# Kernel tuning notes

Hardware: AMD Instinct MI355X
Metric: run time of the kernel (lower is better)

## Reference

```python
import jax, jax.numpy as jnp
import numpy as np

TAU = 2.0       # LIF time constant
ALPHA = 4.0     # spikingjelly Sigmoid surrogate alpha
EPS = 1e-5      # BatchNorm eps
NUM_HEADS = 8

@jax.custom_vjp
def _spike(x):
    return (x >= 0.0).astype(x.dtype)

def _spike_fwd(x):
    return _spike(x), x

def _spike_bwd(x, g):
    s = jax.nn.sigmoid(ALPHA * x)
    return (g * ALPHA * s * (1.0 - s),)

_spike.defvjp(_spike_fwd, _spike_bwd)

def lif(x, v_th=1.0):
    """Multi-step LIF over leading time axis. v <- v + (x - v)/tau; hard reset to 0.
    detach_reset=True: spike in reset path is stop-gradient'ed."""
    def step(v, xt):
        v = v + (xt - v) / TAU
        s = _spike(v - v_th)
        v = v * (1.0 - jax.lax.stop_gradient(s))
        return v, s
    _, out = jax.lax.scan(step, jnp.zeros_like(x[0]), x)
    return out

def conv_bn(x, w, gamma, beta, mean, var, bias=None):
    """1x1 Conv1d over channel dim + BatchNorm1d (inference-style, running stats).
    x: [T,B,C,N], w: [Cout,Cin]."""
    y = jnp.einsum('tbcn,dc->tbdn', x, w)
    if bias is not None:
        y = y + bias[None, None, :, None]
    inv = gamma * jax.lax.rsqrt(var + EPS)
    return (y - mean[None, None, :, None]) * inv[None, None, :, None] + beta[None, None, :, None]

def _bn_params(key, C):
    k1, k2, k3 = jax.random.split(key, 3)
    gamma = 1.0 + 0.1 * jax.random.normal(k1, (C,), jnp.float32)
    beta = 0.1 * jax.random.normal(k2, (C,), jnp.float32)
    mean = 0.1 * jax.random.normal(k3, (C,), jnp.float32)
    var = jnp.ones((C,), jnp.float32)
    return gamma, beta, mean, var

def setup_inputs() -> dict:
    key = jax.random.key(0)
    ks = jax.random.split(key, 10)
    T, B, C, N = 4, 8, 512, 1024
    scale = 1.0 / np.sqrt(C)
    d = {}
    d['q'] = jax.random.normal(ks[0], (T, B, C, N), jnp.float32)
    d['k'] = jax.random.normal(ks[1], (T, B, C, N), jnp.float32)
    d['q_w'] = jax.random.normal(ks[2], (C, C), jnp.float32) * scale
    d['k_w'] = jax.random.normal(ks[3], (C, C), jnp.float32) * scale
    d['proj_w'] = jax.random.normal(ks[4], (C, C), jnp.float32) * scale
    d['proj_b'] = 0.01 * jax.random.normal(ks[5], (C,), jnp.float32)
    d['q_gamma'], d['q_beta'], d['q_mean'], d['q_var'] = _bn_params(ks[6], C)
    d['k_gamma'], d['k_beta'], d['k_mean'], d['k_var'] = _bn_params(ks[7], C)
    d['proj_gamma'], d['proj_beta'], d['proj_mean'], d['proj_var'] = _bn_params(ks[8], C)
    return d

def reference(q, k, q_w, k_w, proj_w, proj_b,
              q_gamma, q_beta, q_mean, q_var,
              k_gamma, k_beta, k_mean, k_var,
              proj_gamma, proj_beta, proj_mean, proj_var):
    T, B, C, N = q.shape
    H = NUM_HEADS
    Dh = C // H
    # Q path: conv1x1 + BN + LIF spikes, split heads
    q_s = lif(conv_bn(q, q_w, q_gamma, q_beta, q_mean, q_var))          # [T,B,C,N]
    q_h = q_s.reshape(T, B, H, Dh, N)
    # K path
    k_s = lif(conv_bn(k, k_w, k_gamma, k_beta, k_mean, k_var))          # [T,B,C,N]
    k_h = k_s.reshape(T, B, H, Dh, N)
    # Sum-pool Q over head_dim, spike-gate (threshold 0.5), multiply into K
    q_sum = jnp.sum(q_h, axis=3, keepdims=True)                         # [T,B,H,1,N]
    attn = lif(q_sum, v_th=0.5)                                         # [T,B,H,1,N]
    x = (attn * k_h).reshape(T, B, C, N)
    # Projection: conv1x1 (with bias) + BN + LIF
    x = conv_bn(x, proj_w, proj_gamma, proj_beta, proj_mean, proj_var, bias=proj_b)
    return lif(x)
```

## Files before the change

### kernel.cpp

```cpp
#include <hip/hip_runtime.h>
#include <hip/hip_fp16.h>
#include <stdint.h>

#define TT 4
#define BB 8
#define CC 512
#define NN 1024
#define HH 8

typedef unsigned char u8;
typedef _Float16 f16x8 __attribute__((ext_vector_type(8)));
typedef float f32x16 __attribute__((ext_vector_type(16)));

#define WF_BYTES ((size_t)2*64*512*16)
#define SZ_SPIKE ((size_t)TT*BB*CC*NN)
#define SZ_GATE  ((size_t)TT*BB*HH*NN)

union U4H { uint4 u; f16x8 v; };
__device__ __forceinline__ f16x8 ash(uint4 u){ U4H x; x.u = u; return x.v; }

#define MFMA_F16(a,b,c) __builtin_amdgcn_mfma_f32_32x32x16_f16((a),(b),(c),0,0,0)

__device__ __forceinline__ void gld_lds16(const void* g, void* l){
  __builtin_amdgcn_global_load_lds((const __attribute__((address_space(1))) void*)g,
                                   (__attribute__((address_space(3))) void*)l, 16, 0, 0);
}
__device__ __forceinline__ void gld_lds4(const void* g, void* l){
  __builtin_amdgcn_global_load_lds((const __attribute__((address_space(1))) void*)g,
                                   (__attribute__((address_space(3))) void*)l, 4, 0, 0);
}

#define WAITVM(N) asm volatile("s_waitcnt vmcnt(" #N ")" ::: "memory")
#define WAITLGKM0 asm volatile("s_waitcnt lgkmcnt(0)" ::: "memory")
#define SBAR() __builtin_amdgcn_s_barrier()
#define VMFENCE() asm volatile("" ::: "memory")

__device__ __forceinline__ void split16(float xs, uint32_t& h, uint32_t& m){
  __half hh = __float2half(xs);
  float hf = __half2float(hh);
  __half mm = __float2half(xs - hf);
  h = __half_as_ushort(hh);
  m = __half_as_ushort(mm);
}

__global__ __launch_bounds__(256)
void k_prep(const float* __restrict__ W0, const float* __restrict__ W1,
            const float* __restrict__ W2,
            u8* __restrict__ D0, u8* __restrict__ D1, u8* __restrict__ D2)
{
  const int which = blockIdx.y;
  const float* W = (which == 0) ? W0 : (which == 1) ? W1 : W2;
  u8* D = (which == 0) ? D0 : (which == 1) ? D1 : D2;
  const int tg  = blockIdx.x * 256 + threadIdx.x;
  const int row = tg >> 6;
  const int kh  = tg & 63;
  uint32_t Hw[4], Mw[4];
#pragma unroll
  for (int p = 0; p < 4; ++p){
    uint32_t h0, m0, h1, m1;
    split16(W[row * CC + kh * 8 + 2*p    ] * 64.0f, h0, m0);
    split16(W[row * CC + kh * 8 + 2*p + 1] * 64.0f, h1, m1);
    Hw[p] = h0 | (h1 << 16);
    Mw[p] = m0 | (m1 << 16);
  }
  *(uint4*)(D + ((size_t)(0*64 + kh)*512 + row) * 16) = make_uint4(Hw[0],Hw[1],Hw[2],Hw[3]);
  *(uint4*)(D + ((size_t)(1*64 + kh)*512 + row) * 16) = make_uint4(Mw[0],Mw[1],Mw[2],Mw[3]);
}

__global__ __launch_bounds__(256, 2)
void k_qk(const float* __restrict__ Q, const float* __restrict__ K,
          const u8* __restrict__ WFq, const u8* __restrict__ WFk,
          const float* __restrict__ qg, const float* __restrict__ qb,
          const float* __restrict__ qm, const float* __restrict__ qv,
          const float* __restrict__ kg, const float* __restrict__ kb,
          const float* __restrict__ km, const float* __restrict__ kv,
          u8* __restrict__ Sk, u8* __restrict__ Aa)
{
  __shared__ float xf32[3][4096];
  __shared__ uint4 frag[1024];

  const int hw = blockIdx.x;
  const int lg = (hw & 7) * 128 + (hw >> 3);
  const int d0t  = lg & 1;
  const int n0i  = (lg >> 1) & 31;
  const int b    = (lg >> 6) & 7;
  const int path = (lg >> 9) & 1;
  const int n0 = n0i << 5, d0 = d0t << 8;
  const float* X = path ? K : Q;
  const u8* WF = path ? WFk : WFq;

  const int tid = threadIdx.x, lane = tid & 63, wid = tid >> 6;
  const int hi = lane >> 5, ln31 = lane & 31;

  f32x16 acc[4][2];
#pragma unroll
  for (int t = 0; t < 4; ++t)
#pragma unroll
    for (int rt = 0; rt < 2; ++rt)
#pragma unroll
      for (int r = 0; r < 16; ++r) acc[t][rt][r] = 0.0f;

  uint4 A0[8], A1[8];

  auto stageX = [&](int h, int buf){
    const float* xb = X + ((size_t)(wid*BB + b)*CC + h*32)*NN + n0;
#pragma unroll
    for (int i = 0; i < 4; ++i){
      gld_lds16(xb + (size_t)(i*8 + (lane >> 3))*NN + ((lane & 7) << 2),
                (void*)&xf32[buf][(wid*32 + i*8)*32]);
    }
  };
  auto loadA = [&](uint4* A, int h){
#pragma unroll
    for (int s = 0; s < 2; ++s)
#pragma unroll
      for (int ks = 0; ks < 2; ++ks)
#pragma unroll
        for (int rt = 0; rt < 2; ++rt)
          A[s*4 + ks*2 + rt] = *(const uint4*)(WF +
              ((size_t)(s*64 + h*4 + ks*2 + hi)*512
               + d0 + wid*64 + rt*32 + ln31) * 16);
  };
  auto dosplit = [&](int sb){
    const int c = tid & 127;
    const int t = c >> 5, n = c & 31;
    const int k0 = (tid >> 7) << 4;
    const float* xs = &xf32[sb][(t*32 + k0)*32 + n];
    uint32_t hw_[8], mw_[8];
#pragma unroll
    for (int p = 0; p < 8; ++p){
      uint32_t ha, ma, hb2, mb2;
      split16(xs[(2*p  )*32] * 512.0f, ha, ma);
      split16(xs[(2*p+1)*32] * 512.0f, hb2, mb2);
      hw_[p] = ha | (hb2 << 16);
      mw_[p] = ma | (mb2 << 16);
    }
    const int kb0 = k0 >> 3;
    frag[(kb0    )*128 + c] = make_uint4(hw_[0],hw_[1],hw_[2],hw_[3]);
    frag[(kb0 + 1)*128 + c] = make_uint4(hw_[4],hw_[5],hw_[6],hw_[7]);
    frag[(4 + kb0    )*128 + c] = make_uint4(mw_[0],mw_[1],mw_[2],mw_[3]);
    frag[(4 + kb0 + 1)*128 + c] = make_uint4(mw_[4],mw_[5],mw_[6],mw_[7]);
  };
  auto mstep = [&](const uint4* A){
#pragma unroll
    for (int ks = 0; ks < 2; ++ks){
      const int kbi = ks*2 + hi;
#pragma unroll
      for (int ct = 0; ct < 4; ++ct){
        const int fb = ct*32 + ln31;
        f16x8 bh = ash(frag[kbi*128 + fb]);
        f16x8 bm = ash(frag[(4 + kbi)*128 + fb]);
#pragma unroll
        for (int rt = 0; rt < 2; ++rt){
          acc[ct][rt] = MFMA_F16(ash(A[0*4 + ks*2 + rt]), bh, acc[ct][rt]);
          acc[ct][rt] = MFMA_F16(ash(A[1*4 + ks*2 + rt]), bh, acc[ct][rt]);
          acc[ct][rt] = MFMA_F16(ash(A[0*4 + ks*2 + rt]), bm, acc[ct][rt]);
        }
      }
    }
  };

#define QK_PH(H, VM) { \
    WAITVM(VM); SBAR(); \
    if ((H) < 15) { loadA(((H)&1) ? A0 : A1, (H)+1); VMFENCE(); } \
    if ((H) < 14) { stageX((H)+2, ((H)+2)%3); VMFENCE(); } \
    dosplit((H)%3); \
    WAITLGKM0; SBAR(); \
    mstep(((H)&1) ? A1 : A0); }

  stageX(0, 0); VMFENCE(); stageX(1, 1); VMFENCE(); loadA(A0, 0);
  QK_PH(0,12)  QK_PH(1,12)  QK_PH(2,12)  QK_PH(3,12)
  QK_PH(4,12)  QK_PH(5,12)  QK_PH(6,12)  QK_PH(7,12)
  QK_PH(8,12)  QK_PH(9,12)  QK_PH(10,12) QK_PH(11,12)
  QK_PH(12,12) QK_PH(13,12) QK_PH(14,12) QK_PH(15,8)
#undef QK_PH

  const float* gamma = path ? kg : qg;
  const float* beta  = path ? kb : qb;
  const float* mean  = path ? km : qm;
  const float* var   = path ? kv : qv;

  uint32_t orb = 0;
#pragma unroll
  for (int rt = 0; rt < 2; ++rt)
#pragma unroll
    for (int rg = 0; rg < 4; ++rg){
      const int dbase = d0 + wid*64 + rt*32 + rg*8 + hi*4;
      const float4 g4 = *(const float4*)&gamma[dbase];
      const float4 b4 = *(const float4*)&beta[dbase];
      const float4 m4 = *(const float4*)&mean[dbase];
      const float4 v4 = *(const float4*)&var[dbase];
      const float* gp = (const float*)&g4;
      const float* bp = (const float*)&b4;
      const float* mp = (const float*)&m4;
      const float* vp = (const float*)&v4;
#pragma unroll
      for (int j = 0; j < 4; ++j){
        const float inv = gp[j] * (1.0f / sqrtf(vp[j] + 1e-5f));
        const float c1 = inv * (1.0f/32768.0f);
        const float c0 = bp[j] - mp[j]*inv;
        const int r = rg*4 + j;
        float v = 0.f;
#pragma unroll
        for (int t = 0; t < 4; ++t){
          const float y = fmaf(acc[t][rt][r], c1, c0);
          v = 0.5f*(v + y);
          const bool s = (v >= 1.0f);
          if (s) v = 0.f;
          if (path == 1)
            Sk[((size_t)(t*BB + b)*CC + dbase + j)*NN + n0 + ln31] = (u8)s;
          else
            orb |= ((uint32_t)s) << t;
        }
      }
    }

  if (path == 0){
    orb |= __shfl_xor(orb, 32);
    if (hi == 0){
      const int h = d0t*4 + wid;
#pragma unroll
      for (int t = 0; t < 4; ++t)
        Aa[((size_t)(t*BB + b)*HH + h)*NN + n0 + ln31] = (u8)((orb >> t) & 1);
    }
  }
}

__global__ __launch_bounds__(256, 2)
void k_proj(const u8* __restrict__ Sk, const u8* __restrict__ Ag,
            const u8* __restrict__ WF, const float* __restrict__ bias,
            const float* __restrict__ gamma, const float* __restrict__ beta,
            const float* __restrict__ mean, const float* __restrict__ var,
            float* __restrict__ O)
{
  __shared__ u8   xu[3][8192];
  __shared__ uint4 frag[1024];

  const int hw = blockIdx.x;
  const int lg = (hw & 7) * 64 + (hw >> 3);
  const int d0t = lg & 1;
  const int n0i = (lg >> 1) & 31;
  const int b   = (lg >> 6) & 7;
  const int n0 = n0i << 5, d0 = d0t << 8;

  const int tid = threadIdx.x, lane = tid & 63, wid = tid >> 6;
  const int hi = lane >> 5, ln31 = lane & 31;

  const int st_kh = tid >> 5, st_t = (tid >> 3) & 3, st_n4 = tid & 7;

  f32x16 acc[4][2];
#pragma unroll
  for (int t = 0; t < 4; ++t)
#pragma unroll
    for (int rt = 0; rt < 2; ++rt)
#pragma unroll
      for (int r = 0; r < 16; ++r) acc[t][rt][r] = 0.0f;

  uint4 Ap[16];
  uint32_t gword[8];
#pragma unroll
  for (int p = 0; p < 8; ++p)
    gword[p] = *(const uint32_t*)(Ag +
        ((size_t)(st_t*BB + b)*HH + p)*NN + n0 + st_n4*4);

  auto xustage = [&](int h, int buf){
#pragma unroll
    for (int i = 0; i < 8; ++i){
      const u8* g = Sk + ((size_t)((wid*BB + b)*CC) + (size_t)(h*64 + i*8 + (lane >> 3)))*NN
                       + n0 + (lane & 7)*4;
      gld_lds4(g, (void*)&xu[buf][(wid*64 + i*8)*32]);
    }
  };
  auto loadPA = [&](int p){
#pragma unroll
    for (int s = 0; s < 2; ++s)
#pragma unroll
      for (int ks = 0; ks < 4; ++ks)
#pragma unroll
        for (int rt = 0; rt < 2; ++rt)
          Ap[(s*4 + ks)*2 + rt] = *(const uint4*)(WF +
              ((size_t)(s*64 + p*8 + ks*2 + hi)*512
               + d0 + wid*64 + rt*32 + ln31) * 16);
  };
  auto stage2 = [&](int buf, uint32_t g32){
    uint32_t r[8];
#pragma unroll
    for (int c = 0; c < 8; ++c)
      r[c] = *(const uint32_t*)&xu[buf][(st_t*64 + st_kh*8 + c)*32 + st_n4*4];
#pragma unroll
    for (int j = 0; j < 4; ++j){
      const uint32_t gm   = __builtin_amdgcn_perm(g32, g32, (uint32_t)j * 0x01010101u);
      const uint32_t selp = (uint32_t)j | (((uint32_t)j + 4u) << 8);
      uint32_t p01 = __builtin_amdgcn_perm(r[1], r[0], selp);
      uint32_t p23 = __builtin_amdgcn_perm(r[3], r[2], selp);
      uint32_t p45 = __builtin_amdgcn_perm(r[5], r[4], selp);
      uint32_t p67 = __builtin_amdgcn_perm(r[7], r[6], selp);
      uint32_t lo  = __builtin_amdgcn_perm(p23, p01, 0x05040100u) & gm;
      uint32_t hi_ = __builtin_amdgcn_perm(p67, p45, 0x05040100u) & gm;
      uint32_t w[4];
#pragma unroll
      for (int p = 0; p < 4; ++p){
        const uint32_t src = (p < 2) ? lo : hi_;
        const uint32_t b0 = (src >> ((p & 1) * 16)) & 0xFFu;
        const uint32_t b1 = (src >> ((p & 1) * 16 + 8)) & 0xFFu;
        w[p] = (b0 ? 0x3C00u : 0u) | (b1 ? 0x3C000000u : 0u);
      }
      frag[st_kh*128 + st_t*32 + st_n4*4 + j] = make_uint4(w[0], w[1], w[2], w[3]);
    }
  };
  auto mstepP = [&](){
#pragma unroll
    for (int ks = 0; ks < 4; ++ks){
      const int kbi = ks*2 + hi;
#pragma unroll
      for (int ct = 0; ct < 4; ++ct){
        const int fb = ct*32 + ln31;
        f16x8 bb = ash(frag[kbi*128 + fb]);
#pragma unroll
        for (int rt = 0; rt < 2; ++rt){
          acc[ct][rt] = MFMA_F16(ash(Ap[(0*4 + ks)*2 + rt]), bb, acc[ct][rt]);
          acc[ct][rt] = MFMA_F16(ash(Ap[(1*4 + ks)*2 + rt]), bb, acc[ct][rt]);
        }
      }
    }
  };

#define PJ_PH(P, VM) { \
    WAITVM(VM); SBAR(); \
    loadPA(P); VMFENCE(); \
    if ((P) < 6) { xustage((P)+2, ((P)+2)%3); VMFENCE(); } \
    stage2((P)%3, gword[P]); \
    WAITLGKM0; SBAR(); \
    mstepP(); }

  xustage(0, 0); VMFENCE(); xustage(1, 1); VMFENCE();
  PJ_PH(0,8) PJ_PH(1,8) PJ_PH(2,8) PJ_PH(3,8)
  PJ_PH(4,8) PJ_PH(5,8) PJ_PH(6,8) PJ_PH(7,0)
#undef PJ_PH

#pragma unroll
  for (int rt = 0; rt < 2; ++rt)
#pragma unroll
    for (int rg = 0; rg < 4; ++rg){
      const int dbase = d0 + wid*64 + rt*32 + rg*8 + hi*4;
      const float4 g4 = *(const float4*)&gamma[dbase];
      const float4 b4 = *(const float4*)&beta[dbase];
      const float4 m4 = *(const float4*)&mean[dbase];
      const float4 v4 = *(const float4*)&var[dbase];
      const float4 s4 = *(const float4*)&bias[dbase];
      const float* gp = (const float*)&g4;
      const float* bp = (const float*)&b4;
      const float* mp = (const float*)&m4;
      const float* vp = (const float*)&v4;
      const float* sp = (const float*)&s4;
#pragma unroll
      for (int j = 0; j < 4; ++j){
        const float inv = gp[j] * (1.0f / sqrtf(vp[j] + 1e-5f));
        const float c1 = inv * (1.0f/64.0f);
        const float c0 = (sp[j] - mp[j])*inv + bp[j];
        const int r = rg*4 + j;
        float v = 0.f;
#pragma unroll
        for (int t = 0; t < 4; ++t){
          const float y = fmaf(acc[t][rt][r], c1, c0);
          v = 0.5f*(v + y);
          const bool s = (v >= 1.0f);
          if (s) v = 0.f;
          O[((size_t)(t*BB + b)*CC + dbase + j)*NN + n0 + ln31] = s ? 1.f : 0.f;
        }
      }
    }
}

extern "C" void kernel_launch(void* const* d_in, const int* in_sizes, int n_in,
                              void* d_out, int out_size, void* d_ws, size_t ws_size,
                              hipStream_t stream)
{
  const float* q   = (const float*)d_in[0];
  const float* k   = (const float*)d_in[1];
  const float* qw  = (const float*)d_in[2];
  const float* kw  = (const float*)d_in[3];
  const float* pw  = (const float*)d_in[4];
  const float* pb  = (const float*)d_in[5];
  const float* qg  = (const float*)d_in[6];
  const float* qbt = (const float*)d_in[7];
  const float* qm  = (const float*)d_in[8];
  const float* qv  = (const float*)d_in[9];
  const float* kg  = (const float*)d_in[10];
  const float* kbt = (const float*)d_in[11];
  const float* km  = (const float*)d_in[12];
  const float* kv  = (const float*)d_in[13];
  const float* pg  = (const float*)d_in[14];
  const float* pbt = (const float*)d_in[15];
  const float* pm  = (const float*)d_in[16];
  const float* pv  = (const float*)d_in[17];

  u8* WFq = (u8*)d_ws;
  u8* WFk = WFq + WF_BYTES;
  u8* WFp = WFk + WF_BYTES;
  u8* Sk  = WFp + WF_BYTES;
  u8* Aa  = Sk + SZ_SPIKE;
  const size_t need = 3*WF_BYTES + SZ_SPIKE + SZ_GATE;
  if (ws_size < need) return;

  k_prep<<<dim3(128, 3), 256, 0, stream>>>(qw, kw, pw, WFq, WFk, WFp);
  k_qk<<<1024, 256, 0, stream>>>(q, k, WFq, WFk,
                                 qg, qbt, qm, qv, kg, kbt, km, kv, Sk, Aa);
  k_proj<<<512, 256, 0, stream>>>(Sk, Aa, WFp, pb, pg, pbt, pm, pv, (float*)d_out);
}
```

Baseline: 163.5 us.

## Widen QK tile to all 512 output channels and load X through registers

Each block of the Q/K conv kernel now computes all 512 output channels for its 32-column slice, instead of splitting the channels across two blocks. This halves the grid and means each X element is read and split into f16 parts only once rather than twice. The LDS fp32 staging via global_load_lds is replaced by direct per-thread global loads into registers, a double-buffered fragment array, and a simpler one-barrier-per-phase pipeline. The accumulator count doubles and occupancy is lowered to one block per CU, so latency hiding may suffer and the register-loaded strided X reads may coalesce worse.

```diff
diff --git a/kernel.cpp b/kernel.cpp
--- a/kernel.cpp
+++ b/kernel.cpp
@@ -21,10 +21,6 @@
 
 #define MFMA_F16(a,b,c) __builtin_amdgcn_mfma_f32_32x32x16_f16((a),(b),(c),0,0,0)
 
-__device__ __forceinline__ void gld_lds16(const void* g, void* l){
-  __builtin_amdgcn_global_load_lds((const __attribute__((address_space(1))) void*)g,
-                                   (__attribute__((address_space(3))) void*)l, 16, 0, 0);
-}
 __device__ __forceinline__ void gld_lds4(const void* g, void* l){
   __builtin_amdgcn_global_load_lds((const __attribute__((address_space(1))) void*)g,
                                    (__attribute__((address_space(3))) void*)l, 4, 0, 0);
@@ -67,7 +63,7 @@
   *(uint4*)(D + ((size_t)(1*64 + kh)*512 + row) * 16) = make_uint4(Mw[0],Mw[1],Mw[2],Mw[3]);
 }
 
-__global__ __launch_bounds__(256, 2)
+__global__ __launch_bounds__(256, 1)
 void k_qk(const float* __restrict__ Q, const float* __restrict__ K,
           const u8* __restrict__ WFq, const u8* __restrict__ WFk,
           const float* __restrict__ qg, const float* __restrict__ qb,
@@ -76,103 +72,103 @@
           const float* __restrict__ km, const float* __restrict__ kv,
           u8* __restrict__ Sk, u8* __restrict__ Aa)
 {
-  __shared__ float xf32[3][4096];
-  __shared__ uint4 frag[1024];
+  __shared__ uint4 frag[2][1024];
 
   const int hw = blockIdx.x;
-  const int lg = (hw & 7) * 128 + (hw >> 3);
-  const int d0t  = lg & 1;
-  const int n0i  = (lg >> 1) & 31;
-  const int b    = (lg >> 6) & 7;
-  const int path = (lg >> 9) & 1;
-  const int n0 = n0i << 5, d0 = d0t << 8;
+  const int lg = (hw & 7) * 64 + (hw >> 3);
+  const int n0i  = lg & 31;
+  const int b    = (lg >> 5) & 7;
+  const int path = (lg >> 8) & 1;
+  const int n0 = n0i << 5;
   const float* X = path ? K : Q;
   const u8* WF = path ? WFk : WFq;
 
   const int tid = threadIdx.x, lane = tid & 63, wid = tid >> 6;
   const int hi = lane >> 5, ln31 = lane & 31;
 
-  f32x16 acc[4][2];
-#pragma unroll
-  for (int t = 0; t < 4; ++t)
-#pragma unroll
-    for (int rt = 0; rt < 2; ++rt)
-#pragma unroll
-      for (int r = 0; r < 16; ++r) acc[t][rt][r] = 0.0f;
-
-  uint4 A0[8], A1[8];
-
-  auto stageX = [&](int h, int buf){
-    const float* xb = X + ((size_t)(wid*BB + b)*CC + h*32)*NN + n0;
-#pragma unroll
-    for (int i = 0; i < 4; ++i){
-      gld_lds16(xb + (size_t)(i*8 + (lane >> 3))*NN + ((lane & 7) << 2),
-                (void*)&xf32[buf][(wid*32 + i*8)*32]);
-    }
-  };
-  auto loadA = [&](uint4* A, int h){
+  const int c  = tid & 127;
+  const int kq = tid >> 7;
+  const int ct_t = c >> 5, nn = c & 31;
+  const float* Xb = X + ((size_t)(ct_t*BB + b)*CC)*NN + n0 + nn;
+
+  f32x16 acc[4][4];
+#pragma unroll
+  for (int i = 0; i < 4; ++i)
+#pragma unroll
+    for (int j = 0; j < 4; ++j)
+#pragma unroll
+      for (int r = 0; r < 16; ++r) acc[i][j][r] = 0.0f;
+
+  uint4 A[16];
+  float xb[2][16];
+
+  auto loadA = [&](int H){
 #pragma unroll
     for (int s = 0; s < 2; ++s)
 #pragma unroll
       for (int ks = 0; ks < 2; ++ks)
 #pragma unroll
-        for (int rt = 0; rt < 2; ++rt)
-          A[s*4 + ks*2 + rt] = *(const uint4*)(WF +
-              ((size_t)(s*64 + h*4 + ks*2 + hi)*512
-               + d0 + wid*64 + rt*32 + ln31) * 16);
-  };
-  auto dosplit = [&](int sb){
-    const int c = tid & 127;
-    const int t = c >> 5, n = c & 31;
-    const int k0 = (tid >> 7) << 4;
-    const float* xs = &xf32[sb][(t*32 + k0)*32 + n];
+        for (int rt = 0; rt < 4; ++rt)
+          A[(s*2 + ks)*4 + rt] = *(const uint4*)(WF +
+              ((size_t)(s*64 + H*4 + ks*2 + hi)*512
+               + wid*128 + rt*32 + ln31) * 16);
+  };
+  auto loadX = [&](int ktile, float* xr){
+    const float* xp = Xb + (size_t)(ktile*32 + kq*16)*NN;
+#pragma unroll
+    for (int j = 0; j < 16; ++j) xr[j] = xp[(size_t)j*NN];
+  };
+  auto split_write = [&](const float* xr, int fb){
     uint32_t hw_[8], mw_[8];
 #pragma unroll
     for (int p = 0; p < 8; ++p){
       uint32_t ha, ma, hb2, mb2;
-      split16(xs[(2*p  )*32] * 512.0f, ha, ma);
-      split16(xs[(2*p+1)*32] * 512.0f, hb2, mb2);
+      split16(xr[2*p    ] * 512.0f, ha, ma);
+      split16(xr[2*p + 1] * 512.0f, hb2, mb2);
       hw_[p] = ha | (hb2 << 16);
       mw_[p] = ma | (mb2 << 16);
     }
-    const int kb0 = k0 >> 3;
-    frag[(kb0    )*128 + c] = make_uint4(hw_[0],hw_[1],hw_[2],hw_[3]);
-    frag[(kb0 + 1)*128 + c] = make_uint4(hw_[4],hw_[5],hw_[6],hw_[7]);
-    frag[(4 + kb0    )*128 + c] = make_uint4(mw_[0],mw_[1],mw_[2],mw_[3]);
-    frag[(4 + kb0 + 1)*128 + c] = make_uint4(mw_[4],mw_[5],mw_[6],mw_[7]);
-  };
-  auto mstep = [&](const uint4* A){
+    frag[fb][(kq*2    )*128 + c] = make_uint4(hw_[0],hw_[1],hw_[2],hw_[3]);
+    frag[fb][(kq*2 + 1)*128 + c] = make_uint4(hw_[4],hw_[5],hw_[6],hw_[7]);
+    frag[fb][(4 + kq*2    )*128 + c] = make_uint4(mw_[0],mw_[1],mw_[2],mw_[3]);
+    frag[fb][(4 + kq*2 + 1)*128 + c] = make_uint4(mw_[4],mw_[5],mw_[6],mw_[7]);
+  };
+  auto mstep = [&](int fb){
 #pragma unroll
     for (int ks = 0; ks < 2; ++ks){
       const int kbi = ks*2 + hi;
 #pragma unroll
       for (int ct = 0; ct < 4; ++ct){
-        const int fb = ct*32 + ln31;
-        f16x8 bh = ash(frag[kbi*128 + fb]);
-        f16x8 bm = ash(frag[(4 + kbi)*128 + fb]);
-#pragma unroll
-        for (int rt = 0; rt < 2; ++rt){
-          acc[ct][rt] = MFMA_F16(ash(A[0*4 + ks*2 + rt]), bh, acc[ct][rt]);
-          acc[ct][rt] = MFMA_F16(ash(A[1*4 + ks*2 + rt]), bh, acc[ct][rt]);
-          acc[ct][rt] = MFMA_F16(ash(A[0*4 + ks*2 + rt]), bm, acc[ct][rt]);
+        f16x8 bh = ash(frag[fb][kbi*128 + ct*32 + ln31]);
+        f16x8 bm = ash(frag[fb][(4 + kbi)*128 + ct*32 + ln31]);
+#pragma unroll
+        for (int rt = 0; rt < 4; ++rt){
+          acc[ct][rt] = MFMA_F16(ash(A[(0*2 + ks)*4 + rt]), bh, acc[ct][rt]);
+          acc[ct][rt] = MFMA_F16(ash(A[(1*2 + ks)*4 + rt]), bh, acc[ct][rt]);
+          acc[ct][rt] = MFMA_F16(ash(A[(0*2 + ks)*4 + rt]), bm, acc[ct][rt]);
         }
       }
     }
   };
 
-#define QK_PH(H, VM) { \
-    WAITVM(VM); SBAR(); \
-    if ((H) < 15) { loadA(((H)&1) ? A0 : A1, (H)+1); VMFENCE(); } \
-    if ((H) < 14) { stageX((H)+2, ((H)+2)%3); VMFENCE(); } \
-    dosplit((H)%3); \
-    WAITLGKM0; SBAR(); \
-    mstep(((H)&1) ? A1 : A0); }
-
-  stageX(0, 0); VMFENCE(); stageX(1, 1); VMFENCE(); loadA(A0, 0);
-  QK_PH(0,12)  QK_PH(1,12)  QK_PH(2,12)  QK_PH(3,12)
-  QK_PH(4,12)  QK_PH(5,12)  QK_PH(6,12)  QK_PH(7,12)
-  QK_PH(8,12)  QK_PH(9,12)  QK_PH(10,12) QK_PH(11,12)
-  QK_PH(12,12) QK_PH(13,12) QK_PH(14,12) QK_PH(15,8)
+#define QK_PH(H, XL, XN, FC, FN) { \
+    loadA(H); VMFENCE(); \
+    loadX((H)+2, xb[XN]); VMFENCE(); \
+    split_write(xb[XL], FN); \
+    mstep(FC); \
+    WAITLGKM0; SBAR(); }
+
+  loadX(0, xb[0]); VMFENCE();
+  loadX(1, xb[1]); VMFENCE();
+  split_write(xb[0], 0);
+  WAITLGKM0; SBAR();
+
+  for (int Hb = 0; Hb < 14; Hb += 2){
+    QK_PH(Hb,     1, 0, 0, 1)
+    QK_PH(Hb + 1, 0, 1, 1, 0)
+  }
+  { loadA(14); VMFENCE(); split_write(xb[1], 1); mstep(0); WAITLGKM0; SBAR(); }
+  { loadA(15); VMFENCE(); mstep(1); }
 #undef QK_PH
 
   const float* gamma = path ? kg : qg;
@@ -180,12 +176,12 @@
   const float* mean  = path ? km : qm;
   const float* var   = path ? kv : qv;
 
-  uint32_t orb = 0;
-#pragma unroll
-  for (int rt = 0; rt < 2; ++rt)
+  uint32_t orb[2] = {0, 0};
+#pragma unroll
+  for (int rt = 0; rt < 4; ++rt)
 #pragma unroll
     for (int rg = 0; rg < 4; ++rg){
-      const int dbase = d0 + wid*64 + rt*32 + rg*8 + hi*4;
+      const int dbase = wid*128 + rt*32 + rg*8 + hi*4;
       const float4 g4 = *(const float4*)&gamma[dbase];
       const float4 b4 = *(const float4*)&beta[dbase];
       const float4 m4 = *(const float4*)&mean[dbase];
@@ -210,18 +206,21 @@
           if (path == 1)
             Sk[((size_t)(t*BB + b)*CC + dbase + j)*NN + n0 + ln31] = (u8)s;
           else
-            orb |= ((uint32_t)s) << t;
+            orb[rt >> 1] |= ((uint32_t)s) << t;
         }
       }
     }
 
   if (path == 0){
-    orb |= __shfl_xor(orb, 32);
+    orb[0] |= __shfl_xor(orb[0], 32);
+    orb[1] |= __shfl_xor(orb[1], 32);
     if (hi == 0){
-      const int h = d0t*4 + wid;
-#pragma unroll
-      for (int t = 0; t < 4; ++t)
-        Aa[((size_t)(t*BB + b)*HH + h)*NN + n0 + ln31] = (u8)((orb >> t) & 1);
+#pragma unroll
+      for (int hh = 0; hh < 2; ++hh)
+#pragma unroll
+        for (int t = 0; t < 4; ++t)
+          Aa[((size_t)(t*BB + b)*HH + wid*2 + hh)*NN + n0 + ln31] =
+              (u8)((orb[hh] >> t) & 1);
     }
   }
 }
@@ -285,8 +284,8 @@
   auto stage2 = [&](int buf, uint32_t g32){
     uint32_t r[8];
 #pragma unroll
-    for (int c = 0; c < 8; ++c)
-      r[c] = *(const uint32_t*)&xu[buf][(st_t*64 + st_kh*8 + c)*32 + st_n4*4];
+    for (int cc = 0; cc < 8; ++cc)
+      r[cc] = *(const uint32_t*)&xu[buf][(st_t*64 + st_kh*8 + cc)*32 + st_n4*4];
 #pragma unroll
     for (int j = 0; j < 4; ++j){
       const uint32_t gm   = __builtin_amdgcn_perm(g32, g32, (uint32_t)j * 0x01010101u);
@@ -404,7 +403,7 @@
   if (ws_size < need) return;
 
   k_prep<<<dim3(128, 3), 256, 0, stream>>>(qw, kw, pw, WFq, WFk, WFp);
-  k_qk<<<1024, 256, 0, stream>>>(q, k, WFq, WFk,
-                                 qg, qbt, qm, qv, kg, kbt, km, kv, Sk, Aa);
+  k_qk<<<512, 256, 0, stream>>>(q, k, WFq, WFk,
+                                qg, qbt, qm, qv, kg, kbt, km, kv, Sk, Aa);
   k_proj<<<512, 256, 0, stream>>>(Sk, Aa, WFp, pb, pg, pbt, pm, pv, (float*)d_out);
 }
```

After: 182.2 us. 1.11x slower.
